# Optimization experiments

Measured on AMD Instinct MI355X. Metric: run time of the kernel, lower is better.

## Reference

```python
import jax, jax.numpy as jnp
import numpy as np

B, T, C, H = 4, 2048, 1024, 16
D = C // H  # head_dim = 64

def setup_inputs() -> dict:
    key = jax.random.key(0)
    k1, k2, k3 = jax.random.split(key, 3)
    x = jax.random.normal(k1, (B, T, C), dtype=jnp.float32)
    w_qkv = jax.random.normal(k2, (C, 3 * C), dtype=jnp.float32) * (C ** -0.5)
    w_proj = jax.random.normal(k3, (C, C), dtype=jnp.float32) * (C ** -0.5)
    b_proj = jnp.zeros((C,), dtype=jnp.float32)
    return {"x": x, "w_qkv": w_qkv, "w_proj": w_proj, "b_proj": b_proj}

def reference(x, w_qkv, w_proj, b_proj):
    Bx, Tx, Cx = x.shape
    qkv = x @ w_qkv  # [B,T,3C]
    q, k, v = jnp.split(qkv, 3, axis=-1)
    # [B,T,H,D] -> [B,H,T,D]
    q = q.reshape(Bx, Tx, H, D).transpose(0, 2, 1, 3)
    k = k.reshape(Bx, Tx, H, D).transpose(0, 2, 1, 3)
    v = v.reshape(Bx, Tx, H, D).transpose(0, 2, 1, 3)
    scale = 1.0 / np.sqrt(D).astype(np.float32)
    att = jnp.einsum('bhqd,bhkd->bhqk', q, k) * scale  # [B,H,T,T]
    causal = jnp.tril(jnp.ones((Tx, Tx), dtype=bool))
    att = jnp.where(causal, att, -jnp.inf)
    att = jax.nn.softmax(att, axis=-1)
    y = jnp.einsum('bhqk,bhkd->bhqd', att, v)  # [B,H,T,D]
    y = y.transpose(0, 2, 1, 3).reshape(Bx, Tx, Cx)
    return y @ w_proj + b_proj
```

## Files before the change

kernel.cpp:

```cpp
#include <hip/hip_runtime.h>

typedef unsigned short u16;
typedef unsigned int u32;
typedef __attribute__((ext_vector_type(8))) short bf16x8;
typedef __attribute__((ext_vector_type(4))) float f32x4;
typedef __attribute__((ext_vector_type(16))) float f32x16;
typedef __attribute__((ext_vector_type(4))) unsigned short u16x4;

#define MFMA16(a, b, c) __builtin_amdgcn_mfma_f32_16x16x32_bf16((a), (b), (c), 0, 0, 0)
#define MFMA32(a, b, c) __builtin_amdgcn_mfma_f32_32x32x16_bf16((a), (b), (c), 0, 0, 0)

__device__ __forceinline__ u16 f2bf(float f) {
  union { float f; unsigned int i; } v; v.f = f;
  return (u16)((v.i + 0x7FFFu + ((v.i >> 16) & 1u)) >> 16);
}
__device__ __forceinline__ float exp2a(float x) {
  float r; asm("v_exp_f32 %0, %1" : "=v"(r) : "v"(x)); return r;
}
__device__ __forceinline__ u32 cvtpk(float lo, float hi) {
  u32 d; asm("v_cvt_pk_bf16_f32 %0, %1, %2" : "=v"(d) : "v"(lo), "v"(hi)); return d;
}

__global__ __launch_bounds__(256) void k_transpose(const float* __restrict__ src,
                                                   u16* __restrict__ dst, int R, int C) {
  __shared__ u16 tile[64][65];
  const int c0 = blockIdx.x * 64, r0 = blockIdx.y * 64;
  const int t = threadIdx.x;
#pragma unroll
  for (int i = 0; i < 16; ++i) {
    int e = i * 256 + t, rr = e >> 6, cc = e & 63;
    tile[rr][cc] = f2bf(src[(size_t)(r0 + rr) * C + c0 + cc]);
  }
  __syncthreads();
#pragma unroll
  for (int i = 0; i < 16; ++i) {
    int e = i * 256 + t, rr = e >> 6, cc = e & 63;
    dst[(size_t)(c0 + rr) * R + r0 + cc] = tile[cc][rr];
  }
}

template <int QKV>
__global__ __launch_bounds__(256) void k_gemm(
    const void* __restrict__ Ap, const u16* __restrict__ Bt,
    const float* __restrict__ bias, float* __restrict__ Cf,
    u16* __restrict__ Qb, u16* __restrict__ Kb, u16* __restrict__ VTb,
    int M, int N, int K) {
  __shared__ __attribute__((aligned(16))) u16 As[128 * 32];
  __shared__ __attribute__((aligned(16))) u16 Bs[128 * 32];
  const int bn = blockIdx.x, bm = blockIdx.y;
  const int t = threadIdx.x, lane = t & 63, w = t >> 6;
  const int wr = w >> 1, wc = w & 1;
  const int rh = lane & 15, kg = lane >> 4;

  f32x4 acc[4][4];
#pragma unroll
  for (int mi = 0; mi < 4; ++mi)
#pragma unroll
    for (int ni = 0; ni < 4; ++ni) acc[mi][ni] = (f32x4)0.0f;

  for (int k0 = 0; k0 < K; k0 += 32) {
#pragma unroll
    for (int i = 0; i < 2; ++i) {
      int c = t + 256 * i;
      int r = c >> 2, c8 = (c & 3) << 3;
      if (QKV) {
        const float* s = (const float*)Ap + (size_t)(bm * 128 + r) * K + k0 + c8;
        float4 a = *(const float4*)s;
        float4 b4 = *(const float4*)(s + 4);
        union { u16 e[8]; int4 v; } u;
        u.e[0] = f2bf(a.x); u.e[1] = f2bf(a.y); u.e[2] = f2bf(a.z); u.e[3] = f2bf(a.w);
        u.e[4] = f2bf(b4.x); u.e[5] = f2bf(b4.y); u.e[6] = f2bf(b4.z); u.e[7] = f2bf(b4.w);
        *(int4*)(&As[r * 32 + c8]) = u.v;
      } else {
        const u16* s = (const u16*)Ap + (size_t)(bm * 128 + r) * K + k0 + c8;
        *(int4*)(&As[r * 32 + c8]) = *(const int4*)s;
      }
      const u16* sb = Bt + (size_t)(bn * 128 + r) * K + k0 + c8;
      *(int4*)(&Bs[r * 32 + c8]) = *(const int4*)sb;
    }
    __syncthreads();
    bf16x8 af[4], bfr[4];
#pragma unroll
    for (int mi = 0; mi < 4; ++mi)
      af[mi] = *(const bf16x8*)(&As[(wr * 64 + mi * 16 + rh) * 32 + kg * 8]);
#pragma unroll
    for (int ni = 0; ni < 4; ++ni)
      bfr[ni] = *(const bf16x8*)(&Bs[(wc * 64 + ni * 16 + rh) * 32 + kg * 8]);
#pragma unroll
    for (int mi = 0; mi < 4; ++mi)
#pragma unroll
      for (int ni = 0; ni < 4; ++ni)
        acc[mi][ni] = MFMA16(af[mi], bfr[ni], acc[mi][ni]);
    __syncthreads();
  }

  if (QKV == 0) {
    const int rbase = bm * 128 + wr * 64;
    const int cbase = bn * 128 + wc * 64;
#pragma unroll
    for (int ni = 0; ni < 4; ++ni) {
      const int col = cbase + ni * 16 + rh;
      const float bv = bias ? bias[col] : 0.0f;
#pragma unroll
      for (int mi = 0; mi < 4; ++mi) {
#pragma unroll
        for (int r = 0; r < 4; ++r) {
          int row = rbase + mi * 16 + kg * 4 + r;
          Cf[(size_t)row * N + col] = acc[mi][ni][r] + bv;
        }
      }
    }
  } else {
    const float SCQ = 0.125f * 1.44269504f;
    const int rowbase = bm * 128 + wr * 64;
    const int b = rowbase >> 11;
    const int tb = rowbase & 2047;
    const int cbase = bn * 128 + wc * 64;
    const int role = cbase >> 10;
    const int h = (cbase & 1023) >> 6;
    const int bh = b * 16 + h;
#pragma unroll
    for (int ni = 0; ni < 4; ++ni) {
      const int d = ni * 16 + rh;
#pragma unroll
      for (int mi = 0; mi < 4; ++mi) {
        const int tt = tb + mi * 16 + kg * 4;
        if (role == 2) {
          u16x4 pk;
#pragma unroll
          for (int r = 0; r < 4; ++r) pk[r] = f2bf(acc[mi][ni][r]);
          *(u16x4*)(&VTb[((size_t)bh * 64 + d) * 2048 + tt]) = pk;
        } else {
          u16* dst = (role == 0) ? Qb : Kb;
          const float sc = (role == 0) ? SCQ : 1.0f;
#pragma unroll
          for (int r = 0; r < 4; ++r)
            dst[((size_t)bh * 2048 + tt + r) * 64 + d] = f2bf(acc[mi][ni][r] * sc);
        }
      }
    }
  }
}

__global__ __launch_bounds__(128, 2) void k_attn(const u16* __restrict__ Qb,
                                                 const u16* __restrict__ Kb,
                                                 const u16* __restrict__ VTb,
                                                 u16* __restrict__ Y) {
  const int bh = blockIdx.x;
  const int w = threadIdx.x >> 6;
  const int sb = w ? 31 - (int)blockIdx.y : (int)blockIdx.y;
  const int lane = threadIdx.x & 63;
  const int q31 = lane & 31, hi = lane >> 5;
  const int qA = sb * 64 + q31;
  const int qBr = sb * 64 + 32 + q31;
  const u16* Qh = Qb + (size_t)bh * 2048 * 64;
  const u16* Kh = Kb + (size_t)bh * 2048 * 64;
  const u16* Vh = VTb + (size_t)bh * 64 * 2048;
  const int b = bh >> 4, h = bh & 15;

  bf16x8 qfA[4], qfB[4];
#pragma unroll
  for (int d = 0; d < 4; ++d) {
    qfA[d] = *(const bf16x8*)(&Qh[(size_t)qA * 64 + d * 16 + hi * 8]);
    qfB[d] = *(const bf16x8*)(&Qh[(size_t)qBr * 64 + d * 16 + hi * 8]);
  }

  f32x16 oA0 = (f32x16)0.0f, oA1 = (f32x16)0.0f;
  f32x16 oB0 = (f32x16)0.0f, oB1 = (f32x16)0.0f;
  float mA = -1e30f, sA = 0.0f, mB = -1e30f, sB = 0.0f;

  const int nt = 2 * sb + 2;
  for (int tt = 0; tt < nt; ++tt) {
    const int j0 = tt * 32;
    const bool aAct = tt < nt - 1;

    bf16x8 kf[4];
#pragma unroll
    for (int d = 0; d < 4; ++d)
      kf[d] = *(const bf16x8*)(&Kh[(size_t)(j0 + q31) * 64 + d * 16 + hi * 8]);
    const bf16x8 vf0 = *(const bf16x8*)(&Vh[(size_t)q31 * 2048 + j0 + hi * 8]);
    const bf16x8 vf1 = *(const bf16x8*)(&Vh[(size_t)q31 * 2048 + j0 + 16 + hi * 8]);
    const bf16x8 vf2 = *(const bf16x8*)(&Vh[(size_t)(32 + q31) * 2048 + j0 + hi * 8]);
    const bf16x8 vf3 = *(const bf16x8*)(&Vh[(size_t)(32 + q31) * 2048 + j0 + 16 + hi * 8]);

    f32x16 stB = (f32x16)0.0f;
    __builtin_amdgcn_s_setprio(1);
#pragma unroll
    for (int d = 0; d < 4; ++d) stB = MFMA32(kf[d], qfB[d], stB);
    f32x16 stA = (f32x16)0.0f;
    if (aAct) {
#pragma unroll
      for (int d = 0; d < 4; ++d) stA = MFMA32(kf[d], qfA[d], stA);
    }
    __builtin_amdgcn_s_setprio(0);

    if (tt == nt - 2) {
#pragma unroll
      for (int r = 0; r < 16; ++r) {
        const int kcol = (r & 3) + 8 * (r >> 2) + 4 * hi;
        if (kcol > q31) stA[r] = -1e30f;
      }
    }
    if (tt == nt - 1) {
#pragma unroll
      for (int r = 0; r < 16; ++r) {
        const int kcol = (r & 3) + 8 * (r >> 2) + 4 * hi;
        if (kcol > q31) stB[r] = -1e30f;
      }
    }

    union { u32 w4[4]; bf16x8 f; } paA0, paA1, paB0, paB1;
    if (aAct) {
      float mx = fmaxf(
          fmaxf(fmaxf(fmaxf(stA[0], stA[1]), fmaxf(stA[2], stA[3])),
                fmaxf(fmaxf(stA[4], stA[5]), fmaxf(stA[6], stA[7]))),
          fmaxf(fmaxf(fmaxf(stA[8], stA[9]), fmaxf(stA[10], stA[11])),
                fmaxf(fmaxf(stA[12], stA[13]), fmaxf(stA[14], stA[15]))));
      if (__any(mx - mA > 8.0f)) {
        mx = fmaxf(mx, __shfl_xor(mx, 32));
        const float mn = fmaxf(mA, mx);
        const float scf = exp2a(mA - mn);
        mA = mn; sA *= scf; oA0 *= scf; oA1 *= scf;
      }
      float p[16];
#pragma unroll
      for (int r = 0; r < 16; ++r) p[r] = exp2a(stA[r] - mA);
      sA += (((p[0] + p[1]) + (p[2] + p[3])) + ((p[4] + p[5]) + (p[6] + p[7]))) +
            (((p[8] + p[9]) + (p[10] + p[11])) + ((p[12] + p[13]) + (p[14] + p[15])));
      u32 D0 = cvtpk(p[0], p[1]),   D1 = cvtpk(p[2], p[3]);
      u32 D2 = cvtpk(p[4], p[5]),   D3 = cvtpk(p[6], p[7]);
      u32 D4 = cvtpk(p[8], p[9]),   D5 = cvtpk(p[10], p[11]);
      u32 D6 = cvtpk(p[12], p[13]), D7 = cvtpk(p[14], p[15]);
      u32 X0 = __shfl_xor(D0, 32), X1 = __shfl_xor(D1, 32);
      u32 X2 = __shfl_xor(D2, 32), X3 = __shfl_xor(D3, 32);
      u32 X4 = __shfl_xor(D4, 32), X5 = __shfl_xor(D5, 32);
      u32 X6 = __shfl_xor(D6, 32), X7 = __shfl_xor(D7, 32);
      paA0.w4[0] = hi ? X2 : D0; paA0.w4[1] = hi ? X3 : D1;
      paA0.w4[2] = hi ? D2 : X0; paA0.w4[3] = hi ? D3 : X1;
      paA1.w4[0] = hi ? X6 : D4; paA1.w4[1] = hi ? X7 : D5;
      paA1.w4[2] = hi ? D6 : X4; paA1.w4[3] = hi ? D7 : X5;
    }

    {
      float mx = fmaxf(
          fmaxf(fmaxf(fmaxf(stB[0], stB[1]), fmaxf(stB[2], stB[3])),
                fmaxf(fmaxf(stB[4], stB[5]), fmaxf(stB[6], stB[7]))),
          fmaxf(fmaxf(fmaxf(stB[8], stB[9]), fmaxf(stB[10], stB[11])),
                fmaxf(fmaxf(stB[12], stB[13]), fmaxf(stB[14], stB[15]))));
      if (__any(mx - mB > 8.0f)) {
        mx = fmaxf(mx, __shfl_xor(mx, 32));
        const float mn = fmaxf(mB, mx);
        const float scf = exp2a(mB - mn);
        mB = mn; sB *= scf; oB0 *= scf; oB1 *= scf;
      }
      float p[16];
#pragma unroll
      for (int r = 0; r < 16; ++r) p[r] = exp2a(stB[r] - mB);
      sB += (((p[0] + p[1]) + (p[2] + p[3])) + ((p[4] + p[5]) + (p[6] + p[7]))) +
            (((p[8] + p[9]) + (p[10] + p[11])) + ((p[12] + p[13]) + (p[14] + p[15])));
      u32 D0 = cvtpk(p[0], p[1]),   D1 = cvtpk(p[2], p[3]);
      u32 D2 = cvtpk(p[4], p[5]),   D3 = cvtpk(p[6], p[7]);
      u32 D4 = cvtpk(p[8], p[9]),   D5 = cvtpk(p[10], p[11]);
      u32 D6 = cvtpk(p[12], p[13]), D7 = cvtpk(p[14], p[15]);
      u32 X0 = __shfl_xor(D0, 32), X1 = __shfl_xor(D1, 32);
      u32 X2 = __shfl_xor(D2, 32), X3 = __shfl_xor(D3, 32);
      u32 X4 = __shfl_xor(D4, 32), X5 = __shfl_xor(D5, 32);
      u32 X6 = __shfl_xor(D6, 32), X7 = __shfl_xor(D7, 32);
      paB0.w4[0] = hi ? X2 : D0; paB0.w4[1] = hi ? X3 : D1;
      paB0.w4[2] = hi ? D2 : X0; paB0.w4[3] = hi ? D3 : X1;
      paB1.w4[0] = hi ? X6 : D4; paB1.w4[1] = hi ? X7 : D5;
      paB1.w4[2] = hi ? D6 : X4; paB1.w4[3] = hi ? D7 : X5;
    }

    __builtin_amdgcn_s_setprio(1);
    oB0 = MFMA32(vf0, paB0.f, oB0);
    oB0 = MFMA32(vf1, paB1.f, oB0);
    oB1 = MFMA32(vf2, paB0.f, oB1);
    oB1 = MFMA32(vf3, paB1.f, oB1);
    if (aAct) {
      oA0 = MFMA32(vf0, paA0.f, oA0);
      oA0 = MFMA32(vf1, paA1.f, oA0);
      oA1 = MFMA32(vf2, paA0.f, oA1);
      oA1 = MFMA32(vf3, paA1.f, oA1);
    }
    __builtin_amdgcn_s_setprio(0);
  }

  sA += __shfl_xor(sA, 32);
  sB += __shfl_xor(sB, 32);
  const float invA = 1.0f / sA, invB = 1.0f / sB;
  u16* yrowA = Y + ((size_t)b * 2048 + qA) * 1024 + h * 64;
  u16* yrowB = Y + ((size_t)b * 2048 + qBr) * 1024 + h * 64;
#pragma unroll
  for (int a = 0; a < 4; ++a) {
    u16x4 pk;
#pragma unroll
    for (int i = 0; i < 4; ++i) pk[i] = f2bf(oA0[a * 4 + i] * invA);
    *(u16x4*)(yrowA + a * 8 + 4 * hi) = pk;
#pragma unroll
    for (int i = 0; i < 4; ++i) pk[i] = f2bf(oA1[a * 4 + i] * invA);
    *(u16x4*)(yrowA + 32 + a * 8 + 4 * hi) = pk;
#pragma unroll
    for (int i = 0; i < 4; ++i) pk[i] = f2bf(oB0[a * 4 + i] * invB);
    *(u16x4*)(yrowB + a * 8 + 4 * hi) = pk;
#pragma unroll
    for (int i = 0; i < 4; ++i) pk[i] = f2bf(oB1[a * 4 + i] * invB);
    *(u16x4*)(yrowB + 32 + a * 8 + 4 * hi) = pk;
  }
}

extern "C" void kernel_launch(void* const* d_in, const int* in_sizes, int n_in,
                              void* d_out, int out_size, void* d_ws, size_t ws_size,
                              hipStream_t stream) {
  const float* x      = (const float*)d_in[0];
  const float* w_qkv  = (const float*)d_in[1];
  const float* w_proj = (const float*)d_in[2];
  const float* b_proj = (const float*)d_in[3];
  float* out = (float*)d_out;

  char* ws = (char*)d_ws;
  u16* wqkvT  = (u16*)(ws);
  u16* wprojT = (u16*)(ws + 6291456);
  u16* Qb     = (u16*)(ws + 8388608);
  u16* Kb     = (u16*)(ws + 25165824);
  u16* VTb    = (u16*)(ws + 41943040);
  u16* Yb     = (u16*)(ws + 58720256);

  k_transpose<<<dim3(48, 16), 256, 0, stream>>>(w_qkv, wqkvT, 1024, 3072);
  k_transpose<<<dim3(16, 16), 256, 0, stream>>>(w_proj, wprojT, 1024, 1024);
  k_gemm<1><<<dim3(24, 64), 256, 0, stream>>>(x, wqkvT, nullptr, nullptr,
                                              Qb, Kb, VTb, 8192, 3072, 1024);
  k_attn<<<dim3(64, 16), 128, 0, stream>>>(Qb, Kb, VTb, (u16*)Yb);
  k_gemm<0><<<dim3(8, 64), 256, 0, stream>>>(Yb, wprojT, b_proj, out,
                                             nullptr, nullptr, nullptr, 8192, 1024, 1024);
}
```

Baseline: 216.6 us.

## Pre-convert x to bf16 and load GEMM tiles via direct global-to-LDS loads

A new kernel converts x to bf16 once, instead of each QKV GEMM block converting fp32 on the fly. This removes repeated fp32 reads and conversions across the 24 column blocks. Both GEMMs now stage A and B tiles with global_load_lds 16-byte direct-to-LDS loads, skipping the register round trip, and raise wave priority around the MFMA loop. The cost is an extra launch and an extra pass over x, and the Y buffer now reuses the xb workspace.

```diff
diff --git a/kernel.cpp b/kernel.cpp
--- a/kernel.cpp
+++ b/kernel.cpp
@@ -20,6 +20,24 @@
 __device__ __forceinline__ u32 cvtpk(float lo, float hi) {
   u32 d; asm("v_cvt_pk_bf16_f32 %0, %1, %2" : "=v"(d) : "v"(lo), "v"(hi)); return d;
 }
+__device__ __forceinline__ void gl2lds16(const u16* g, u16* l) {
+  __builtin_amdgcn_global_load_lds(
+      (const __attribute__((address_space(1))) void*)g,
+      (__attribute__((address_space(3))) void*)l, 16, 0, 0);
+}
+
+__global__ __launch_bounds__(256) void k_ingest(const float* __restrict__ src,
+                                                u16* __restrict__ dst, int n8) {
+  const int i = blockIdx.x * 256 + threadIdx.x;
+  if (i >= n8) return;
+  const float* s = src + (size_t)i * 8;
+  float4 a = *(const float4*)(s);
+  float4 b = *(const float4*)(s + 4);
+  union { u16 o[8]; int4 v; } u;
+  u.o[0] = f2bf(a.x); u.o[1] = f2bf(a.y); u.o[2] = f2bf(a.z); u.o[3] = f2bf(a.w);
+  u.o[4] = f2bf(b.x); u.o[5] = f2bf(b.y); u.o[6] = f2bf(b.z); u.o[7] = f2bf(b.w);
+  *(int4*)(&dst[(size_t)i * 8]) = u.v;
+}
 
 __global__ __launch_bounds__(256) void k_transpose(const float* __restrict__ src,
                                                    u16* __restrict__ dst, int R, int C) {
@@ -41,7 +59,7 @@
 
 template <int QKV>
 __global__ __launch_bounds__(256) void k_gemm(
-    const void* __restrict__ Ap, const u16* __restrict__ Bt,
+    const u16* __restrict__ A, const u16* __restrict__ Bt,
     const float* __restrict__ bias, float* __restrict__ Cf,
     u16* __restrict__ Qb, u16* __restrict__ Kb, u16* __restrict__ VTb,
     int M, int N, int K) {
@@ -51,6 +69,7 @@
   const int t = threadIdx.x, lane = t & 63, w = t >> 6;
   const int wr = w >> 1, wc = w & 1;
   const int rh = lane & 15, kg = lane >> 4;
+  const int srow = lane >> 2, sk8 = (lane & 3) << 3;
 
   f32x4 acc[4][4];
 #pragma unroll
@@ -61,24 +80,13 @@
   for (int k0 = 0; k0 < K; k0 += 32) {
 #pragma unroll
     for (int i = 0; i < 2; ++i) {
-      int c = t + 256 * i;
-      int r = c >> 2, c8 = (c & 3) << 3;
-      if (QKV) {
-        const float* s = (const float*)Ap + (size_t)(bm * 128 + r) * K + k0 + c8;
-        float4 a = *(const float4*)s;
-        float4 b4 = *(const float4*)(s + 4);
-        union { u16 e[8]; int4 v; } u;
-        u.e[0] = f2bf(a.x); u.e[1] = f2bf(a.y); u.e[2] = f2bf(a.z); u.e[3] = f2bf(a.w);
-        u.e[4] = f2bf(b4.x); u.e[5] = f2bf(b4.y); u.e[6] = f2bf(b4.z); u.e[7] = f2bf(b4.w);
-        *(int4*)(&As[r * 32 + c8]) = u.v;
-      } else {
-        const u16* s = (const u16*)Ap + (size_t)(bm * 128 + r) * K + k0 + c8;
-        *(int4*)(&As[r * 32 + c8]) = *(const int4*)s;
-      }
-      const u16* sb = Bt + (size_t)(bn * 128 + r) * K + k0 + c8;
-      *(int4*)(&Bs[r * 32 + c8]) = *(const int4*)sb;
-    }
+      const int r0 = w * 32 + i * 16;
+      gl2lds16(&A[(size_t)(bm * 128 + r0 + srow) * K + k0 + sk8], &As[r0 * 32]);
+      gl2lds16(&Bt[(size_t)(bn * 128 + r0 + srow) * K + k0 + sk8], &Bs[r0 * 32]);
+    }
+    asm volatile("s_waitcnt vmcnt(0)" ::: "memory");
     __syncthreads();
+
     bf16x8 af[4], bfr[4];
 #pragma unroll
     for (int mi = 0; mi < 4; ++mi)
@@ -86,11 +94,13 @@
 #pragma unroll
     for (int ni = 0; ni < 4; ++ni)
       bfr[ni] = *(const bf16x8*)(&Bs[(wc * 64 + ni * 16 + rh) * 32 + kg * 8]);
+    __builtin_amdgcn_s_setprio(1);
 #pragma unroll
     for (int mi = 0; mi < 4; ++mi)
 #pragma unroll
       for (int ni = 0; ni < 4; ++ni)
         acc[mi][ni] = MFMA16(af[mi], bfr[ni], acc[mi][ni]);
+    __builtin_amdgcn_s_setprio(0);
     __syncthreads();
   }
 
@@ -324,13 +334,15 @@
   u16* Qb     = (u16*)(ws + 8388608);
   u16* Kb     = (u16*)(ws + 25165824);
   u16* VTb    = (u16*)(ws + 41943040);
-  u16* Yb     = (u16*)(ws + 58720256);
-
+  u16* xb     = (u16*)(ws + 58720256);
+  u16* Yb     = xb;
+
+  k_ingest<<<4096, 256, 0, stream>>>(x, xb, 1048576);
   k_transpose<<<dim3(48, 16), 256, 0, stream>>>(w_qkv, wqkvT, 1024, 3072);
   k_transpose<<<dim3(16, 16), 256, 0, stream>>>(w_proj, wprojT, 1024, 1024);
-  k_gemm<1><<<dim3(24, 64), 256, 0, stream>>>(x, wqkvT, nullptr, nullptr,
+  k_gemm<1><<<dim3(24, 64), 256, 0, stream>>>(xb, wqkvT, nullptr, nullptr,
                                               Qb, Kb, VTb, 8192, 3072, 1024);
-  k_attn<<<dim3(64, 16), 128, 0, stream>>>(Qb, Kb, VTb, (u16*)Yb);
+  k_attn<<<dim3(64, 16), 128, 0, stream>>>(Qb, Kb, VTb, Yb);
   k_gemm<0><<<dim3(8, 64), 256, 0, stream>>>(Yb, wprojT, b_proj, out,
                                              nullptr, nullptr, nullptr, 8192, 1024, 1024);
 }
```

Measured after the change: 212.9 us. About the same (-1.7%).
